# Kernel tuning notes

Measured on AMD Instinct MI355X. Metric: run time of the kernel, lower is better.

The kernel has to match this reference:

```python
import jax, jax.numpy as jnp
import numpy as np

EMBED_DIM = 1024
NUM_HEADS = 16
HEAD_DIM = EMBED_DIM // NUM_HEADS
MLP_HIDDEN = 4096
B, S = 2, 2048


def setup_inputs() -> dict:
    key = jax.random.key(0)
    ks = jax.random.split(key, 10)
    sd = lambda fan_in: 1.0 / np.sqrt(fan_in)
    x = jax.random.normal(ks[0], (B, S, EMBED_DIM), dtype=jnp.float32)
    # weights stored (in, out) so y = x @ W + b (same math as torch Linear)
    w_qkv = jax.random.normal(ks[1], (EMBED_DIM, 3 * EMBED_DIM), jnp.float32) * sd(EMBED_DIM)
    w_proj = jax.random.normal(ks[2], (EMBED_DIM, EMBED_DIM), jnp.float32) * sd(EMBED_DIM)
    b_proj = jnp.zeros((EMBED_DIM,), jnp.float32)
    w_fc1 = jax.random.normal(ks[3], (EMBED_DIM, MLP_HIDDEN), jnp.float32) * sd(EMBED_DIM)
    b_fc1 = jnp.zeros((MLP_HIDDEN,), jnp.float32)
    w_fc2 = jax.random.normal(ks[4], (MLP_HIDDEN, EMBED_DIM), jnp.float32) * sd(MLP_HIDDEN)
    b_fc2 = jnp.zeros((EMBED_DIM,), jnp.float32)
    g1 = jnp.ones((EMBED_DIM,), jnp.float32)
    be1 = jnp.zeros((EMBED_DIM,), jnp.float32)
    g2 = jnp.ones((EMBED_DIM,), jnp.float32)
    be2 = jnp.zeros((EMBED_DIM,), jnp.float32)
    return {"x": x, "w_qkv": w_qkv, "w_proj": w_proj, "b_proj": b_proj,
            "w_fc1": w_fc1, "b_fc1": b_fc1, "w_fc2": w_fc2, "b_fc2": b_fc2,
            "g1": g1, "be1": be1, "g2": g2, "be2": be2}


def _layernorm(x, g, b, eps=1e-5):
    mu = jnp.mean(x, axis=-1, keepdims=True)
    var = jnp.var(x, axis=-1, keepdims=True)
    return (x - mu) * jax.lax.rsqrt(var + eps) * g + b


def _block(x, w_qkv, w_proj, b_proj, w_fc1, b_fc1, w_fc2, b_fc2, g1, be1, g2, be2):
    # --- attention branch ---
    h = _layernorm(x, g1, be1)
    qkv = h @ w_qkv  # [B,S,3D]
    qkv = qkv.reshape(B, S, 3, NUM_HEADS, HEAD_DIM).transpose(2, 0, 3, 1, 4)
    q, k, v = qkv[0], qkv[1], qkv[2]  # each [B,H,S,Dh]
    scale = 1.0 / np.sqrt(HEAD_DIM).astype(np.float32)
    dots = jnp.einsum('bhqd,bhkd->bhqk', q, k) * scale  # naive full score matrix
    attn = jax.nn.softmax(dots, axis=-1)
    out = jnp.einsum('bhqk,bhkd->bhqd', attn, v)
    out = out.transpose(0, 2, 1, 3).reshape(B, S, EMBED_DIM)
    x = x + (out @ w_proj + b_proj)
    # --- mlp branch ---
    h2 = _layernorm(x, g2, be2)
    mlp = jax.nn.gelu(h2 @ w_fc1 + b_fc1, approximate=False) @ w_fc2 + b_fc2
    return x + mlp


def reference(x, w_qkv, w_proj, b_proj, w_fc1, b_fc1, w_fc2, b_fc2, g1, be1, g2, be2):
    return _block(x, w_qkv, w_proj, b_proj, w_fc1, b_fc1, w_fc2, b_fc2, g1, be1, g2, be2)
```

## Files before the change

kernel.cpp:

```cpp
#include <hip/hip_runtime.h>

typedef __attribute__((ext_vector_type(8))) short short8;
typedef __attribute__((ext_vector_type(4))) float f32x4;

#define MFMA16(a, b, c) __builtin_amdgcn_mfma_f32_16x16x32_bf16((a), (b), (c), 0, 0, 0)

static __device__ __forceinline__ unsigned short f2bf(float f) {
    unsigned int u = __float_as_uint(f);
    return (unsigned short)((u + 0x7fffu + ((u >> 16) & 1u)) >> 16);
}

static __device__ __forceinline__ void glds16(const unsigned short* g, unsigned short* l) {
    __builtin_amdgcn_global_load_lds(
        (const __attribute__((address_space(1))) unsigned int*)g,
        (__attribute__((address_space(3))) unsigned int*)l, 16, 0, 0);
}

__global__ __launch_bounds__(256) void convt_all_kernel(
    const float* __restrict__ w_qkv, const float* __restrict__ w_proj,
    const float* __restrict__ w_fc1, const float* __restrict__ w_fc2,
    unsigned short* __restrict__ wqkvT, unsigned short* __restrict__ wprojT,
    unsigned short* __restrict__ wfc1T, unsigned short* __restrict__ wfc2T) {
    __shared__ unsigned short Ts[32][33];
    int id = blockIdx.x;
    const float* W; unsigned short* WT; int K, N, bx, by;
    if (id < 3072)      { W = w_qkv;  WT = wqkvT;  K = 1024; N = 3072; bx = id % 96;  by = id / 96; }
    else if (id < 4096) { id -= 3072; W = w_proj; WT = wprojT; K = 1024; N = 1024; bx = id & 31; by = id >> 5; }
    else if (id < 8192) { id -= 4096; W = w_fc1;  WT = wfc1T;  K = 1024; N = 4096; bx = id & 127; by = id >> 7; }
    else                { id -= 8192; W = w_fc2;  WT = wfc2T;  K = 4096; N = 1024; bx = id & 31; by = id >> 5; }
    int t = threadIdx.x;
    int bk = by * 32, bn = bx * 32;
    int r = t >> 3, c = (t & 7) * 4;
    float4 w = *(const float4*)&W[(size_t)(bk + r) * N + bn + c];
    Ts[c + 0][r] = f2bf(w.x); Ts[c + 1][r] = f2bf(w.y);
    Ts[c + 2][r] = f2bf(w.z); Ts[c + 3][r] = f2bf(w.w);
    __syncthreads();
    ushort4 o;
    o.x = Ts[r][c]; o.y = Ts[r][c + 1]; o.z = Ts[r][c + 2]; o.w = Ts[r][c + 3];
    *(ushort4*)&WT[(size_t)(bn + r) * K + bk + c] = o;
}

__global__ __launch_bounds__(256) void ln_kernel(const float* __restrict__ x,
                                                 const float* __restrict__ g,
                                                 const float* __restrict__ be,
                                                 unsigned short* __restrict__ y) {
    int row = blockIdx.x;
    const float* xr = x + (size_t)row * 1024;
    unsigned short* yr = y + (size_t)row * 1024;
    int t = threadIdx.x;
    float v[4];
    float sum = 0.f, sq = 0.f;
#pragma unroll
    for (int i = 0; i < 4; ++i) {
        float f = xr[t + i * 256];
        v[i] = f; sum += f; sq += f * f;
    }
#pragma unroll
    for (int o = 32; o > 0; o >>= 1) { sum += __shfl_down(sum, o); sq += __shfl_down(sq, o); }
    __shared__ float red[8];
    int wave = t >> 6, lane = t & 63;
    if (lane == 0) { red[wave] = sum; red[4 + wave] = sq; }
    __syncthreads();
    sum = red[0] + red[1] + red[2] + red[3];
    sq  = red[4] + red[5] + red[6] + red[7];
    float mean = sum * (1.f / 1024.f);
    float var  = sq * (1.f / 1024.f) - mean * mean;
    float rstd = rsqrtf(var + 1e-5f);
#pragma unroll
    for (int i = 0; i < 4; ++i) {
        int c = t + i * 256;
        yr[c] = f2bf((v[i] - mean) * rstd * g[c] + be[c]);
    }
}

#define PHASE_MID                                            \
    __builtin_amdgcn_sched_barrier(0);                       \
    __builtin_amdgcn_s_barrier();                            \
    asm volatile("s_waitcnt lgkmcnt(0)" ::: "memory");       \
    __builtin_amdgcn_sched_barrier(0);                       \
    __builtin_amdgcn_s_setprio(1);
#define PHASE_END                                            \
    __builtin_amdgcn_s_setprio(0);                           \
    __builtin_amdgcn_sched_barrier(0);                       \
    __builtin_amdgcn_s_barrier();

__global__ __launch_bounds__(512, 2) void gemm256_kernel(const unsigned short* __restrict__ A,
                                                         const unsigned short* __restrict__ BT,
                                                         const float* __restrict__ bias,
                                                         const float* __restrict__ resid,
                                                         void* __restrict__ C,
                                                         int M, int N, int K, int act, int cF32) {
    __shared__ __align__(16) unsigned short As[2][2][256][32];
    __shared__ __align__(16) unsigned short Bs[2][2][256][32];
    int t = threadIdx.x, wave = t >> 6, lane = t & 63;
    int lm = lane & 15, quad = lane >> 4;
    int wm = (wave >> 2) * 128, wn = (wave & 3) * 64;

    int id = blockIdx.y * gridDim.x + blockIdx.x;
    int gsz = gridDim.x * 8;
    int grp = id / gsz, rem = id % gsz;
    int br = (grp * 8 + (rem & 7)) * 256;
    int bc = (rem >> 3) * 256;

    int srow = lane >> 2;
    int scol = ((lane & 3) ^ ((srow >> 1) & 3)) * 8;
    const unsigned short* Ag = A + (size_t)(br + wave * 16 + srow) * K + scol;
    const unsigned short* Bg = BT + (size_t)(bc + wave * 16 + srow) * K + scol;

    auto stA = [&](int p_, int half, int ko) {
        const unsigned short* g = Ag + (size_t)half * 128 * K + ko;
        glds16(g,      &As[p_][0][half * 128 + wave * 16][0]);
        glds16(g + 32, &As[p_][1][half * 128 + wave * 16][0]);
    };
    auto stB = [&](int p_, int half, int ko) {
        const unsigned short* g = Bg + (size_t)half * 128 * K + ko;
        glds16(g,      &Bs[p_][0][half * 128 + wave * 16][0]);
        glds16(g + 32, &Bs[p_][1][half * 128 + wave * 16][0]);
    };

    f32x4 zero4 = {0.f, 0.f, 0.f, 0.f};
    f32x4 acc[8][4];
#pragma unroll
    for (int i = 0; i < 8; ++i)
#pragma unroll
        for (int j = 0; j < 4; ++j) acc[i][j] = zero4;

    int ntile = K >> 6;
    stA(0, 0, 0); stA(0, 1, 0); stB(0, 0, 0); stB(0, 1, 0);
    if (ntile > 1) { stB(1, 0, 64); stA(1, 0, 64); }
    __builtin_amdgcn_sched_barrier(0);
    if (ntile > 1) asm volatile("s_waitcnt vmcnt(4)" ::: "memory");
    else           asm volatile("s_waitcnt vmcnt(0)" ::: "memory");
    __builtin_amdgcn_s_barrier();

    int cq = (quad ^ ((lm >> 1) & 3)) << 3;

    for (int tt = 0; tt < ntile; ++tt) {
        int p = tt & 1, q = p ^ 1;
        int tko = tt * 64;
        short8 aLo0[4], aLo1[4], bLo0[2], bLo1[2];
#pragma unroll
        for (int i = 0; i < 4; ++i) {
            aLo0[i] = *(const short8*)&As[p][0][wm + i * 16 + lm][cq];
            aLo1[i] = *(const short8*)&As[p][1][wm + i * 16 + lm][cq];
        }
#pragma unroll
        for (int j = 0; j < 2; ++j) {
            bLo0[j] = *(const short8*)&Bs[p][0][wn + j * 16 + lm][cq];
            bLo1[j] = *(const short8*)&Bs[p][1][wn + j * 16 + lm][cq];
        }
        if (tt + 1 < ntile) stB(q, 1, tko + 64);
        PHASE_MID;
#pragma unroll
        for (int i = 0; i < 4; ++i)
#pragma unroll
            for (int j = 0; j < 2; ++j) {
                acc[i][j] = MFMA16(aLo0[i], bLo0[j], acc[i][j]);
                acc[i][j] = MFMA16(aLo1[i], bLo1[j], acc[i][j]);
            }
        PHASE_END;
        short8 bHi0[2], bHi1[2];
#pragma unroll
        for (int j = 0; j < 2; ++j) {
            bHi0[j] = *(const short8*)&Bs[p][0][wn + 32 + j * 16 + lm][cq];
            bHi1[j] = *(const short8*)&Bs[p][1][wn + 32 + j * 16 + lm][cq];
        }
        if (tt + 1 < ntile) stA(q, 1, tko + 64);
        PHASE_MID;
#pragma unroll
        for (int i = 0; i < 4; ++i)
#pragma unroll
            for (int j = 0; j < 2; ++j) {
                acc[i][j + 2] = MFMA16(aLo0[i], bHi0[j], acc[i][j + 2]);
                acc[i][j + 2] = MFMA16(aLo1[i], bHi1[j], acc[i][j + 2]);
            }
        PHASE_END;
        short8 aHi0[4], aHi1[4];
#pragma unroll
        for (int i = 0; i < 4; ++i) {
            aHi0[i] = *(const short8*)&As[p][0][wm + 64 + i * 16 + lm][cq];
            aHi1[i] = *(const short8*)&As[p][1][wm + 64 + i * 16 + lm][cq];
        }
        if (tt + 2 < ntile) stB(p, 0, tko + 128);
        PHASE_MID;
#pragma unroll
        for (int i = 0; i < 4; ++i)
#pragma unroll
            for (int j = 0; j < 2; ++j) {
                acc[i + 4][j] = MFMA16(aHi0[i], bLo0[j], acc[i + 4][j]);
                acc[i + 4][j] = MFMA16(aHi1[i], bLo1[j], acc[i + 4][j]);
            }
        PHASE_END;
        if (tt + 2 < ntile) stA(p, 0, tko + 128);
        __builtin_amdgcn_sched_barrier(0);
        if (tt + 2 < ntile) asm volatile("s_waitcnt vmcnt(4)" ::: "memory");
        else                asm volatile("s_waitcnt vmcnt(0)" ::: "memory");
        __builtin_amdgcn_s_barrier();
        asm volatile("s_waitcnt lgkmcnt(0)" ::: "memory");
        __builtin_amdgcn_sched_barrier(0);
        __builtin_amdgcn_s_setprio(1);
#pragma unroll
        for (int i = 0; i < 4; ++i)
#pragma unroll
            for (int j = 0; j < 2; ++j) {
                acc[i + 4][j + 2] = MFMA16(aHi0[i], bHi0[j], acc[i + 4][j + 2]);
                acc[i + 4][j + 2] = MFMA16(aHi1[i], bHi1[j], acc[i + 4][j + 2]);
            }
        PHASE_END;
    }

#pragma unroll
    for (int i = 0; i < 8; ++i)
#pragma unroll
        for (int j = 0; j < 4; ++j) {
            int col = bc + wn + j * 16 + lm;
            float bv = bias ? bias[col] : 0.f;
#pragma unroll
            for (int r = 0; r < 4; ++r) {
                int row = br + wm + i * 16 + quad * 4 + r;
                float v = acc[i][j][r] + bv;
                if (act == 1) v = 0.5f * v * (1.f + erff(v * 0.70710678118f));
                size_t idx = (size_t)row * N + col;
                if (resid) v += resid[idx];
                if (cF32) ((float*)C)[idx] = v;
                else ((unsigned short*)C)[idx] = f2bf(v);
            }
        }
}

__global__ __launch_bounds__(256) void gemm64_4ph(const unsigned short* __restrict__ A,
                                                  const unsigned short* __restrict__ BT,
                                                  const float* __restrict__ bias,
                                                  const float* __restrict__ resid,
                                                  void* __restrict__ C,
                                                  int M, int N, int K, int act, int cF32) {
    __shared__ __align__(16) unsigned short As[3][2][128][32];
    __shared__ __align__(16) unsigned short Bs[3][2][64][32];
    int t = threadIdx.x, wave = t >> 6, lane = t & 63;
    int lm = lane & 15, quad = lane >> 4;
    int wm = (wave >> 1) * 64, wn = (wave & 1) * 32;

    int id = blockIdx.y * gridDim.x + blockIdx.x;
    int gsz = gridDim.x * 8;
    int grp = id / gsz, rem = id % gsz;
    int br = (grp * 8 + (rem & 7)) * 128;
    int bc = (rem >> 3) * 64;

    int srow = lane >> 2;
    int scol = ((lane & 3) ^ ((srow >> 1) & 3)) * 8;
    const unsigned short* Ag = A + (size_t)(br + wave * 16 + srow) * K + scol;
    const unsigned short* Bg = BT + (size_t)(bc + wave * 16 + srow) * K + scol;

    auto stA = [&](int b, int ko) {
#pragma unroll
        for (int l = 0; l < 4; ++l)
            glds16(Ag + (size_t)(l >> 1) * 64 * K + (l & 1) * 32 + ko,
                   &As[b][l & 1][(l >> 1) * 64 + wave * 16][0]);
    };
    auto stB = [&](int b, int ko) {
#pragma unroll
        for (int l = 0; l < 2; ++l)
            glds16(Bg + (size_t)l * 32 + ko, &Bs[b][l][wave * 16][0]);
    };

    f32x4 zero4 = {0.f, 0.f, 0.f, 0.f};
    f32x4 acc[4][2];
#pragma unroll
    for (int i = 0; i < 4; ++i) { acc[i][0] = zero4; acc[i][1] = zero4; }

    int nt = K >> 6;
    stA(0, 0); stB(0, 0);
    if (nt > 1) { stA(1, 64); stB(1, 64); }
    __builtin_amdgcn_sched_barrier(0);
    if (nt > 1) asm volatile("s_waitcnt vmcnt(6)" ::: "memory");
    else        asm volatile("s_waitcnt vmcnt(0)" ::: "memory");
    __builtin_amdgcn_s_barrier();

    int cq = (quad ^ ((lm >> 1) & 3)) << 3;

    int p = 0;
    for (int tt = 0; tt < nt; ++tt) {
        int pn = p + 1; if (pn == 3) pn = 0;
        int pnn = pn + 1; if (pnn == 3) pnn = 0;
        short8 a0[4], a1[4], b00, b01;
#pragma unroll
        for (int i = 0; i < 4; ++i) {
            a0[i] = *(const short8*)&As[p][0][wm + i * 16 + lm][cq];
            a1[i] = *(const short8*)&As[p][1][wm + i * 16 + lm][cq];
        }
        b00 = *(const short8*)&Bs[p][0][wn + lm][cq];
        b01 = *(const short8*)&Bs[p][1][wn + lm][cq];
        if (tt + 2 < nt) stA(pnn, (tt + 2) << 6);
        PHASE_MID;
#pragma unroll
        for (int i = 0; i < 4; ++i) {
            acc[i][0] = MFMA16(a0[i], b00, acc[i][0]);
            acc[i][0] = MFMA16(a1[i], b01, acc[i][0]);
        }
        PHASE_END;
        short8 b10 = *(const short8*)&Bs[p][0][wn + 16 + lm][cq];
        short8 b11 = *(const short8*)&Bs[p][1][wn + 16 + lm][cq];
        if (tt + 2 < nt) stB(pnn, (tt + 2) << 6);
        __builtin_amdgcn_sched_barrier(0);
        if (tt + 2 < nt) asm volatile("s_waitcnt vmcnt(6)" ::: "memory");
        else             asm volatile("s_waitcnt vmcnt(0)" ::: "memory");
        __builtin_amdgcn_s_barrier();
        asm volatile("s_waitcnt lgkmcnt(0)" ::: "memory");
        __builtin_amdgcn_sched_barrier(0);
        __builtin_amdgcn_s_setprio(1);
#pragma unroll
        for (int i = 0; i < 4; ++i) {
            acc[i][1] = MFMA16(a0[i], b10, acc[i][1]);
            acc[i][1] = MFMA16(a1[i], b11, acc[i][1]);
        }
        PHASE_END;
        p = pn;
    }

#pragma unroll
    for (int i = 0; i < 4; ++i)
#pragma unroll
        for (int j = 0; j < 2; ++j) {
            int col = bc + wn + j * 16 + lm;
            float bv = bias ? bias[col] : 0.f;
#pragma unroll
            for (int r = 0; r < 4; ++r) {
                int row = br + wm + i * 16 + quad * 4 + r;
                float v = acc[i][j][r] + bv;
                if (act == 1) v = 0.5f * v * (1.f + erff(v * 0.70710678118f));
                size_t idx = (size_t)row * N + col;
                if (resid) v += resid[idx];
                if (cF32) ((float*)C)[idx] = v;
                else ((unsigned short*)C)[idx] = f2bf(v);
            }
        }
}

template <int BN>
__global__ __launch_bounds__(256) void gemm_kernel(const unsigned short* __restrict__ A,
                                                   const unsigned short* __restrict__ BT,
                                                   const float* __restrict__ bias,
                                                   const float* __restrict__ resid,
                                                   void* __restrict__ C,
                                                   int M, int N, int K, int act, int cF32) {
    constexpr int NT = BN / 32;
    __shared__ __align__(16) unsigned short As[2][128][32];
    __shared__ __align__(16) unsigned short Bs[2][BN][32];
    int t = threadIdx.x, wave = t >> 6, lane = t & 63;
    int lm = lane & 15, quad = lane >> 4;
    int wm = (wave >> 1) * 64, wn = (wave & 1) * (BN / 2);

    int id = blockIdx.y * gridDim.x + blockIdx.x;
    int gsz = gridDim.x * 8;
    int grp = id / gsz, rem = id % gsz;
    int br = (grp * 8 + (rem & 7)) * 128;
    int bc = (rem >> 3) * BN;

    int srow = lane >> 2;
    int scol = ((lane & 3) ^ ((srow >> 1) & 3)) * 8;
    const unsigned short* Ag0 = A + (size_t)(br + wave * 32 + srow) * K + scol;
    const unsigned short* Ag1 = Ag0 + (size_t)16 * K;
    const unsigned short* Bg0 = BT + (size_t)(bc + wave * (BN / 4) + srow) * K + scol;
    const unsigned short* Bg1 = Bg0 + (size_t)16 * K;

    f32x4 zero4 = {0.f, 0.f, 0.f, 0.f};
    f32x4 acc[4][NT];
#pragma unroll
    for (int i = 0; i < 4; ++i)
#pragma unroll
        for (int j = 0; j < NT; ++j) acc[i][j] = zero4;

    auto stage = [&](int buf, int ko) {
        glds16(Ag0 + ko, &As[buf][wave * 32][0]);
        glds16(Ag1 + ko, &As[buf][wave * 32 + 16][0]);
        glds16(Bg0 + ko, &Bs[buf][wave * (BN / 4)][0]);
        if (BN == 128) glds16(Bg1 + ko, &Bs[buf][wave * (BN / 4) + 16][0]);
    };

    int nt = K >> 5;
    stage(0, 0);
    int rsw = (lm >> 1) & 3;
    int cq = (quad ^ rsw) << 3;
    for (int tt = 0; tt < nt; ++tt) {
        int cur = tt & 1;
        if (tt + 1 < nt) {
            stage(cur ^ 1, (tt + 1) << 5);
            if (BN == 128) asm volatile("s_waitcnt vmcnt(4)" ::: "memory");
            else           asm volatile("s_waitcnt vmcnt(3)" ::: "memory");
        } else {
            asm volatile("s_waitcnt vmcnt(0)" ::: "memory");
        }
        __builtin_amdgcn_s_barrier();
        __builtin_amdgcn_sched_barrier(0);
        short8 af[4], bf[NT];
#pragma unroll
        for (int i = 0; i < 4; ++i) af[i] = *(const short8*)&As[cur][wm + i * 16 + lm][cq];
#pragma unroll
        for (int j = 0; j < NT; ++j) bf[j] = *(const short8*)&Bs[cur][wn + j * 16 + lm][cq];
#pragma unroll
        for (int i = 0; i < 4; ++i)
#pragma unroll
            for (int j = 0; j < NT; ++j) acc[i][j] = MFMA16(af[i], bf[j], acc[i][j]);
        __builtin_amdgcn_sched_barrier(0);
        __builtin_amdgcn_s_barrier();
    }

#pragma unroll
    for (int i = 0; i < 4; ++i)
#pragma unroll
        for (int j = 0; j < NT; ++j) {
            int col = bc + wn + j * 16 + lm;
            float bv = bias ? bias[col] : 0.f;
#pragma unroll
            for (int r = 0; r < 4; ++r) {
                int row = br + wm + i * 16 + quad * 4 + r;
                float v = acc[i][j][r] + bv;
                if (act == 1) v = 0.5f * v * (1.f + erff(v * 0.70710678118f));
                size_t idx = (size_t)row * N + col;
                if (resid) v += resid[idx];
                if (cF32) ((float*)C)[idx] = v;
                else ((unsigned short*)C)[idx] = f2bf(v);
            }
        }
}

__global__ __launch_bounds__(256) void kvprep_kernel(const unsigned short* __restrict__ qkv,
                                                     unsigned short* __restrict__ Kp,
                                                     unsigned short* __restrict__ Vt) {
    __shared__ unsigned short Vl[64][72];
    int t = threadIdx.x;
    int w = blockIdx.x, bh = blockIdx.y;
    int b = bh >> 4, h = bh & 15;
    int kt = w * 64;
    int sl = t >> 2, c = (t & 3) * 16;
    const unsigned short* src = qkv + (size_t)(b * 2048 + kt + sl) * 3072 + h * 64 + c;
    {
        uint4 k0 = *(const uint4*)(src + 1024);
        uint4 k1 = *(const uint4*)(src + 1024 + 8);
        int sw = sl & 7;
        int o0 = (c >> 3), o1 = o0 + 1;
        unsigned short* krow = Kp + ((size_t)bh * 2048 + kt + sl) * 64;
        *(uint4*)&krow[(o0 ^ sw) << 3] = k0;
        *(uint4*)&krow[(o1 ^ sw) << 3] = k1;
    }
    {
        uint4 v0 = *(const uint4*)(src + 2048);
        uint4 v1 = *(const uint4*)(src + 2048 + 8);
        *(uint4*)&Vl[sl][c] = v0;
        *(uint4*)&Vl[sl][c + 8] = v1;
    }
    __syncthreads();
    {
        int d = t >> 2, kc = (t & 3) * 16;
        unsigned short vv[16];
#pragma unroll
        for (int i = 0; i < 16; ++i) vv[i] = Vl[kc + i][d];
        int sw = d & 7;
        int ko0 = kc >> 3, ko1 = ko0 + 1;
        unsigned short* vrow = Vt + ((((size_t)bh * 32 + w) * 64) + d) * 64;
        *(uint4*)&vrow[(ko0 ^ sw) << 3] = *(uint4*)&vv[0];
        *(uint4*)&vrow[(ko1 ^ sw) << 3] = *(uint4*)&vv[8];
    }
}

__global__ __launch_bounds__(256) void attn2_kernel(const unsigned short* __restrict__ qkv,
                                                    const unsigned short* __restrict__ Kp,
                                                    const unsigned short* __restrict__ Vt,
                                                    unsigned short* __restrict__ out) {
    __shared__ __align__(16) unsigned short Qs[64][72];
    __shared__ __align__(16) unsigned short Ks[4096];
    __shared__ __align__(16) unsigned short Vs[4096];
    __shared__ __align__(16) unsigned short Ps[4][16][72];

    int t = threadIdx.x, wave = t >> 6, lane = t & 63;
    int lm = lane & 15, quad = lane >> 4, k8 = quad * 8;
    int bh = blockIdx.y, b = bh >> 4, h = bh & 15;
    int q0 = blockIdx.x * 64;
    const unsigned short* base = qkv + (size_t)b * 2048 * 3072 + h * 64;

    {
        int r = t >> 2, c = (t & 3) * 16;
        const unsigned short* src = base + (size_t)(q0 + r) * 3072 + c;
        *(uint4*)&Qs[r][c] = *(const uint4*)src;
        *(uint4*)&Qs[r][c + 8] = *(const uint4*)(src + 8);
    }
    __syncthreads();
    short8 qa0 = *(const short8*)&Qs[wave * 16 + lm][k8];
    short8 qa1 = *(const short8*)&Qs[wave * 16 + lm][32 + k8];

    f32x4 zero4 = {0.f, 0.f, 0.f, 0.f};
    f32x4 oacc[4] = {zero4, zero4, zero4, zero4};
    float lsum[4] = {0.f, 0.f, 0.f, 0.f};

    for (int kt = 0; kt < 2048; kt += 64) {
        __syncthreads();
        {
            const unsigned short* kg = Kp + ((size_t)bh * 2048 + kt) * 64 + wave * 1024 + (lane << 3);
            unsigned short* kl = &Ks[wave * 1024];
            glds16(kg, kl);
            glds16(kg + 512, kl + 512);
            const unsigned short* vg = Vt + (((size_t)bh * 32 + (kt >> 6)) * 64) * 64 + wave * 1024 + (lane << 3);
            unsigned short* vl = &Vs[wave * 1024];
            glds16(vg, vl);
            glds16(vg + 512, vl + 512);
        }
        __syncthreads();

        f32x4 s[4];
        __builtin_amdgcn_s_setprio(1);
#pragma unroll
        for (int nt = 0; nt < 4; ++nt) {
            int key = nt * 16 + lm;
            int swk = lm & 7;
            const unsigned short* krow = &Ks[key * 64];
            short8 kf0 = *(const short8*)&krow[(quad ^ swk) << 3];
            short8 kf1 = *(const short8*)&krow[((quad ^ swk) ^ 4) << 3];
            f32x4 a = zero4;
            a = MFMA16(qa0, kf0, a);
            a = MFMA16(qa1, kf1, a);
            s[nt] = a;
        }
        __builtin_amdgcn_s_setprio(0);

#pragma unroll
        for (int r = 0; r < 4; ++r) {
            int row = quad * 4 + r;
            int sw = (row >> 1) & 7;
#pragma unroll
            for (int nt = 0; nt < 4; ++nt) {
                float p = __expf(s[nt][r] * 0.125f - 8.0f);
                lsum[r] += p;
                int g = (nt << 1) + (lm >> 3);
                Ps[wave][row][((g ^ sw) << 3) + (lm & 7)] = f2bf(p);
            }
        }

        __builtin_amdgcn_s_setprio(1);
#pragma unroll
        for (int kh = 0; kh < 2; ++kh) {
            int pg = (kh << 2) + quad;
            short8 pa = *(const short8*)&Ps[wave][lm][(pg ^ ((lm >> 1) & 7)) << 3];
#pragma unroll
            for (int nt = 0; nt < 4; ++nt) {
                int d = nt * 16 + lm;
                short8 vf = *(const short8*)&Vs[d * 64 + ((pg ^ (lm & 7)) << 3)];
                oacc[nt] = MFMA16(pa, vf, oacc[nt]);
            }
        }
        __builtin_amdgcn_s_setprio(0);
    }

#pragma unroll
    for (int r = 0; r < 4; ++r) {
        float l = lsum[r];
        l += __shfl_xor(l, 1); l += __shfl_xor(l, 2);
        l += __shfl_xor(l, 4); l += __shfl_xor(l, 8);
        float inv = 1.f / l;
        int qrow = q0 + wave * 16 + quad * 4 + r;
        size_t o = ((size_t)(b * 2048 + qrow)) * 1024 + h * 64;
#pragma unroll
        for (int nt = 0; nt < 4; ++nt) out[o + nt * 16 + lm] = f2bf(oacc[nt][r] * inv);
    }
}

__global__ __launch_bounds__(256) void attn_kernel(const unsigned short* __restrict__ qkv,
                                                   unsigned short* __restrict__ out) {
    __shared__ __align__(16) unsigned short Qs[64][72];
    __shared__ __align__(16) unsigned short Ks[64][72];
    __shared__ __align__(16) unsigned short Vs[64][72];
    __shared__ __align__(16) unsigned short Ps[4][16][72];
    int t = threadIdx.x, wave = t >> 6, lane = t & 63;
    int lm = lane & 15, quad = lane >> 4, k8 = quad * 8;
    int bh = blockIdx.y, b = bh >> 4, h = bh & 15;
    int q0 = blockIdx.x * 64;
    const unsigned short* base = qkv + (size_t)b * 2048 * 3072 + h * 64;
    const unsigned short* kb = base + 1024;
    const unsigned short* vb = base + 2048;
    {
        int r = t >> 2, c = (t & 3) * 16;
        const unsigned short* src = base + (size_t)(q0 + r) * 3072 + c;
        *(uint4*)&Qs[r][c] = *(const uint4*)src;
        *(uint4*)&Qs[r][c + 8] = *(const uint4*)(src + 8);
    }
    __syncthreads();
    short8 qa0 = *(const short8*)&Qs[wave * 16 + lm][k8];
    short8 qa1 = *(const short8*)&Qs[wave * 16 + lm][32 + k8];
    f32x4 zero4 = {0.f, 0.f, 0.f, 0.f};
    f32x4 oacc[4] = {zero4, zero4, zero4, zero4};
    float lsum[4] = {0.f, 0.f, 0.f, 0.f};
    int sr = t >> 2, sc = (t & 3) * 16;
    for (int kt = 0; kt < 2048; kt += 64) {
        __syncthreads();
        {
            const unsigned short* ksrc = kb + (size_t)(kt + sr) * 3072 + sc;
            *(uint4*)&Ks[sr][sc] = *(const uint4*)ksrc;
            *(uint4*)&Ks[sr][sc + 8] = *(const uint4*)(ksrc + 8);
            const unsigned short* vsrc = vb + (size_t)(kt + sr) * 3072 + sc;
            unsigned short tv[16] __attribute__((aligned(16)));
            *(uint4*)&tv[0] = *(const uint4*)vsrc;
            *(uint4*)&tv[8] = *(const uint4*)(vsrc + 8);
            int kg = sr >> 3, kw = sr & 7;
#pragma unroll
            for (int j = 0; j < 16; ++j) {
                int d = sc + j;
                Vs[d][((kg ^ ((d >> 3) & 7)) << 3) + kw] = tv[j];
            }
        }
        __syncthreads();
        f32x4 s[4];
#pragma unroll
        for (int nt = 0; nt < 4; ++nt) {
            short8 kf0 = *(const short8*)&Ks[nt * 16 + lm][k8];
            short8 kf1 = *(const short8*)&Ks[nt * 16 + lm][32 + k8];
            f32x4 a = zero4;
            a = MFMA16(qa0, kf0, a);
            a = MFMA16(qa1, kf1, a);
            s[nt] = a;
        }
#pragma unroll
        for (int r = 0; r < 4; ++r) {
            int row = quad * 4 + r;
            int sw = (row >> 1) & 7;
#pragma unroll
            for (int nt = 0; nt < 4; ++nt) {
                float p = __expf(s[nt][r] * 0.125f - 8.0f);
                lsum[r] += p;
                int g = (nt << 1) + (lm >> 3);
                Ps[wave][row][((g ^ sw) << 3) + (lm & 7)] = f2bf(p);
            }
        }
#pragma unroll
        for (int kh = 0; kh < 2; ++kh) {
            int pg = (kh << 2) + quad;
            short8 pa = *(const short8*)&Ps[wave][lm][(pg ^ ((lm >> 1) & 7)) << 3];
#pragma unroll
            for (int nt = 0; nt < 4; ++nt) {
                int d = nt * 16 + lm;
                short8 vf = *(const short8*)&Vs[d][(pg ^ ((d >> 3) & 7)) << 3];
                oacc[nt] = MFMA16(pa, vf, oacc[nt]);
            }
        }
    }
#pragma unroll
    for (int r = 0; r < 4; ++r) {
        float l = lsum[r];
        l += __shfl_xor(l, 1); l += __shfl_xor(l, 2);
        l += __shfl_xor(l, 4); l += __shfl_xor(l, 8);
        float inv = 1.f / l;
        int qrow = q0 + wave * 16 + quad * 4 + r;
        size_t o = ((size_t)(b * 2048 + qrow)) * 1024 + h * 64;
#pragma unroll
        for (int nt = 0; nt < 4; ++nt) out[o + nt * 16 + lm] = f2bf(oacc[nt][r] * inv);
    }
}

extern "C" void kernel_launch(void* const* d_in, const int* in_sizes, int n_in,
                              void* d_out, int out_size, void* d_ws, size_t ws_size,
                              hipStream_t stream) {
    const float* x      = (const float*)d_in[0];
    const float* w_qkv  = (const float*)d_in[1];
    const float* w_proj = (const float*)d_in[2];
    const float* b_proj = (const float*)d_in[3];
    const float* w_fc1  = (const float*)d_in[4];
    const float* b_fc1  = (const float*)d_in[5];
    const float* w_fc2  = (const float*)d_in[6];
    const float* b_fc2  = (const float*)d_in[7];
    const float* g1     = (const float*)d_in[8];
    const float* be1    = (const float*)d_in[9];
    const float* g2     = (const float*)d_in[10];
    const float* be2    = (const float*)d_in[11];
    float* out = (float*)d_out;
    unsigned short* sb = (unsigned short*)d_out;

    char* ws = (char*)d_ws;
    unsigned short* wqkvT  = (unsigned short*)ws;
    unsigned short* wprojT = (unsigned short*)(ws + ((size_t)6u << 20));
    unsigned short* wfc1T  = (unsigned short*)(ws + ((size_t)8u << 20));
    unsigned short* wfc2T  = (unsigned short*)(ws + ((size_t)16u << 20));
    unsigned short* qkv    = (unsigned short*)(ws + ((size_t)24u << 20));

    convt_all_kernel<<<dim3(12288), dim3(256), 0, stream>>>(
        w_qkv, w_proj, w_fc1, w_fc2, wqkvT, wprojT, wfc1T, wfc2T);
    ln_kernel<<<dim3(4096), dim3(256), 0, stream>>>(x, g1, be1, sb);
    gemm256_kernel<<<dim3(12, 16), dim3(512), 0, stream>>>(
        sb, wqkvT, nullptr, nullptr, qkv, 4096, 3072, 1024, 0, 0);

    if (ws_size >= ((size_t)72u << 20)) {
        unsigned short* Kp = (unsigned short*)(ws + ((size_t)48u << 20));
        unsigned short* Vt = (unsigned short*)(ws + ((size_t)56u << 20));
        float*          x2 = (float*)(ws + ((size_t)24u << 20));
        unsigned short* m1 = (unsigned short*)(ws + ((size_t)40u << 20));
        kvprep_kernel<<<dim3(32, 32), dim3(256), 0, stream>>>(qkv, Kp, Vt);
        attn2_kernel<<<dim3(32, 32), dim3(256), 0, stream>>>(qkv, Kp, Vt, sb);
        gemm64_4ph<<<dim3(16, 32), dim3(256), 0, stream>>>(
            sb, wprojT, b_proj, x, x2, 4096, 1024, 1024, 0, 1);
        ln_kernel<<<dim3(4096), dim3(256), 0, stream>>>(x2, g2, be2, sb);
        gemm256_kernel<<<dim3(16, 16), dim3(512), 0, stream>>>(
            sb, wfc1T, b_fc1, nullptr, m1, 4096, 4096, 1024, 1, 0);
        gemm64_4ph<<<dim3(16, 32), dim3(256), 0, stream>>>(
            m1, wfc2T, b_fc2, x2, out, 4096, 1024, 4096, 0, 1);
    } else {
        float*          x2  = (float*)(ws + ((size_t)24u << 20));
        unsigned short* m1c = (unsigned short*)(ws + ((size_t)40u << 20));
        unsigned short* h2  = (unsigned short*)d_out + ((size_t)4u << 20);
        attn_kernel<<<dim3(32, 32), dim3(256), 0, stream>>>(qkv, sb);
        gemm_kernel<64><<<dim3(16, 32), dim3(256), 0, stream>>>(
            sb, wprojT, b_proj, x, x2, 4096, 1024, 1024, 0, 1);
        ln_kernel<<<dim3(4096), dim3(256), 0, stream>>>(x2, g2, be2, h2);
        for (int c = 0; c < 4; ++c) {
            size_t ro = (size_t)c * 1024;
            gemm_kernel<128><<<dim3(32, 8), dim3(256), 0, stream>>>(
                h2 + ro * 1024, wfc1T, b_fc1, nullptr, m1c, 1024, 4096, 1024, 1, 0);
            gemm_kernel<64><<<dim3(16, 8), dim3(256), 0, stream>>>(
                m1c, wfc2T, b_fc2, x2 + ro * 1024, out + ro * 1024, 1024, 1024, 4096, 0, 1);
        }
    }
}
```

Baseline: 396.3 us.

## Replace 256x256 GEMM with 128x256 triple-buffered K=32 pipeline for QKV and FC1

Replaces the 256x256-tile, K=64 four-phase GEMM with a 128x256 tile that walks K in steps of 32 through a three-stage LDS ring. Each iteration issues a single prefetch two stages ahead and runs one MFMA block. Smaller tiles double the block count (192 to 384 for QKV, 256 to 512 for FC1) so the grid fills the CUs better, and launch bounds allow 4 blocks per CU. The cost is less operand reuse per tile and more barriers per unit of K.

```diff
diff --git a/kernel.cpp b/kernel.cpp
--- a/kernel.cpp
+++ b/kernel.cpp
@@ -84,117 +84,65 @@
     __builtin_amdgcn_sched_barrier(0);                       \
     __builtin_amdgcn_s_barrier();
 
-__global__ __launch_bounds__(512, 2) void gemm256_kernel(const unsigned short* __restrict__ A,
-                                                         const unsigned short* __restrict__ BT,
-                                                         const float* __restrict__ bias,
-                                                         const float* __restrict__ resid,
-                                                         void* __restrict__ C,
-                                                         int M, int N, int K, int act, int cF32) {
-    __shared__ __align__(16) unsigned short As[2][2][256][32];
-    __shared__ __align__(16) unsigned short Bs[2][2][256][32];
+__global__ __launch_bounds__(512, 4) void gemm128x256_kernel(
+    const unsigned short* __restrict__ A, const unsigned short* __restrict__ BT,
+    const float* __restrict__ bias, const float* __restrict__ resid,
+    void* __restrict__ C, int M, int N, int K, int act, int cF32) {
+    __shared__ __align__(16) unsigned short As[3][128][32];
+    __shared__ __align__(16) unsigned short Bs[3][256][32];
     int t = threadIdx.x, wave = t >> 6, lane = t & 63;
     int lm = lane & 15, quad = lane >> 4;
-    int wm = (wave >> 2) * 128, wn = (wave & 3) * 64;
+    int wm = (wave >> 2) * 64, wn = (wave & 3) * 64;
 
     int id = blockIdx.y * gridDim.x + blockIdx.x;
     int gsz = gridDim.x * 8;
     int grp = id / gsz, rem = id % gsz;
-    int br = (grp * 8 + (rem & 7)) * 256;
+    int br = (grp * 8 + (rem & 7)) * 128;
     int bc = (rem >> 3) * 256;
 
     int srow = lane >> 2;
     int scol = ((lane & 3) ^ ((srow >> 1) & 3)) * 8;
     const unsigned short* Ag = A + (size_t)(br + wave * 16 + srow) * K + scol;
-    const unsigned short* Bg = BT + (size_t)(bc + wave * 16 + srow) * K + scol;
-
-    auto stA = [&](int p_, int half, int ko) {
-        const unsigned short* g = Ag + (size_t)half * 128 * K + ko;
-        glds16(g,      &As[p_][0][half * 128 + wave * 16][0]);
-        glds16(g + 32, &As[p_][1][half * 128 + wave * 16][0]);
+    const unsigned short* Bg = BT + (size_t)(bc + wave * 32 + srow) * K + scol;
+
+    auto stage = [&](int b, int ko) {
+        glds16(Ag + ko, &As[b][wave * 16][0]);
+        glds16(Bg + ko, &Bs[b][wave * 32][0]);
+        glds16(Bg + (size_t)16 * K + ko, &Bs[b][wave * 32 + 16][0]);
     };
-    auto stB = [&](int p_, int half, int ko) {
-        const unsigned short* g = Bg + (size_t)half * 128 * K + ko;
-        glds16(g,      &Bs[p_][0][half * 128 + wave * 16][0]);
-        glds16(g + 32, &Bs[p_][1][half * 128 + wave * 16][0]);
-    };
 
     f32x4 zero4 = {0.f, 0.f, 0.f, 0.f};
-    f32x4 acc[8][4];
-#pragma unroll
-    for (int i = 0; i < 8; ++i)
+    f32x4 acc[4][4];
+#pragma unroll
+    for (int i = 0; i < 4; ++i)
 #pragma unroll
         for (int j = 0; j < 4; ++j) acc[i][j] = zero4;
 
-    int ntile = K >> 6;
-    stA(0, 0, 0); stA(0, 1, 0); stB(0, 0, 0); stB(0, 1, 0);
-    if (ntile > 1) { stB(1, 0, 64); stA(1, 0, 64); }
+    int nt = K >> 5;
+    stage(0, 0);
+    stage(1, 32);
     __builtin_amdgcn_sched_barrier(0);
-    if (ntile > 1) asm volatile("s_waitcnt vmcnt(4)" ::: "memory");
-    else           asm volatile("s_waitcnt vmcnt(0)" ::: "memory");
+    asm volatile("s_waitcnt vmcnt(3)" ::: "memory");
     __builtin_amdgcn_s_barrier();
 
     int cq = (quad ^ ((lm >> 1) & 3)) << 3;
 
-    for (int tt = 0; tt < ntile; ++tt) {
-        int p = tt & 1, q = p ^ 1;
-        int tko = tt * 64;
-        short8 aLo0[4], aLo1[4], bLo0[2], bLo1[2];
-#pragma unroll
-        for (int i = 0; i < 4; ++i) {
-            aLo0[i] = *(const short8*)&As[p][0][wm + i * 16 + lm][cq];
-            aLo1[i] = *(const short8*)&As[p][1][wm + i * 16 + lm][cq];
-        }
-#pragma unroll
-        for (int j = 0; j < 2; ++j) {
-            bLo0[j] = *(const short8*)&Bs[p][0][wn + j * 16 + lm][cq];
-            bLo1[j] = *(const short8*)&Bs[p][1][wn + j * 16 + lm][cq];
-        }
-        if (tt + 1 < ntile) stB(q, 1, tko + 64);
-        PHASE_MID;
-#pragma unroll
-        for (int i = 0; i < 4; ++i)
-#pragma unroll
-            for (int j = 0; j < 2; ++j) {
-                acc[i][j] = MFMA16(aLo0[i], bLo0[j], acc[i][j]);
-                acc[i][j] = MFMA16(aLo1[i], bLo1[j], acc[i][j]);
-            }
-        PHASE_END;
-        short8 bHi0[2], bHi1[2];
-#pragma unroll
-        for (int j = 0; j < 2; ++j) {
-            bHi0[j] = *(const short8*)&Bs[p][0][wn + 32 + j * 16 + lm][cq];
-            bHi1[j] = *(const short8*)&Bs[p][1][wn + 32 + j * 16 + lm][cq];
-        }
-        if (tt + 1 < ntile) stA(q, 1, tko + 64);
-        PHASE_MID;
-#pragma unroll
-        for (int i = 0; i < 4; ++i)
-#pragma unroll
-            for (int j = 0; j < 2; ++j) {
-                acc[i][j + 2] = MFMA16(aLo0[i], bHi0[j], acc[i][j + 2]);
-                acc[i][j + 2] = MFMA16(aLo1[i], bHi1[j], acc[i][j + 2]);
-            }
-        PHASE_END;
-        short8 aHi0[4], aHi1[4];
-#pragma unroll
-        for (int i = 0; i < 4; ++i) {
-            aHi0[i] = *(const short8*)&As[p][0][wm + 64 + i * 16 + lm][cq];
-            aHi1[i] = *(const short8*)&As[p][1][wm + 64 + i * 16 + lm][cq];
-        }
-        if (tt + 2 < ntile) stB(p, 0, tko + 128);
-        PHASE_MID;
-#pragma unroll
-        for (int i = 0; i < 4; ++i)
-#pragma unroll
-            for (int j = 0; j < 2; ++j) {
-                acc[i + 4][j] = MFMA16(aHi0[i], bLo0[j], acc[i + 4][j]);
-                acc[i + 4][j] = MFMA16(aHi1[i], bLo1[j], acc[i + 4][j]);
-            }
-        PHASE_END;
-        if (tt + 2 < ntile) stA(p, 0, tko + 128);
-        __builtin_amdgcn_sched_barrier(0);
-        if (tt + 2 < ntile) asm volatile("s_waitcnt vmcnt(4)" ::: "memory");
-        else                asm volatile("s_waitcnt vmcnt(0)" ::: "memory");
+    int p = 0;
+    for (int tt = 0; tt < nt; ++tt) {
+        int pnn = p + 2; if (pnn >= 3) pnn -= 3;
+        short8 af[4], bf[4];
+#pragma unroll
+        for (int i = 0; i < 4; ++i) af[i] = *(const short8*)&As[p][wm + i * 16 + lm][cq];
+#pragma unroll
+        for (int j = 0; j < 4; ++j) bf[j] = *(const short8*)&Bs[p][wn + j * 16 + lm][cq];
+        if (tt + 2 < nt) {
+            stage(pnn, (tt + 2) << 5);
+            __builtin_amdgcn_sched_barrier(0);
+            asm volatile("s_waitcnt vmcnt(3)" ::: "memory");
+        } else {
+            __builtin_amdgcn_sched_barrier(0);
+            asm volatile("s_waitcnt vmcnt(0)" ::: "memory");
+        }
         __builtin_amdgcn_s_barrier();
         asm volatile("s_waitcnt lgkmcnt(0)" ::: "memory");
         __builtin_amdgcn_sched_barrier(0);
@@ -202,15 +150,13 @@
 #pragma unroll
         for (int i = 0; i < 4; ++i)
 #pragma unroll
-            for (int j = 0; j < 2; ++j) {
-                acc[i + 4][j + 2] = MFMA16(aHi0[i], bHi0[j], acc[i + 4][j + 2]);
-                acc[i + 4][j + 2] = MFMA16(aHi1[i], bHi1[j], acc[i + 4][j + 2]);
-            }
+            for (int j = 0; j < 4; ++j) acc[i][j] = MFMA16(af[i], bf[j], acc[i][j]);
         PHASE_END;
-    }
-
-#pragma unroll
-    for (int i = 0; i < 8; ++i)
+        p = p + 1; if (p == 3) p = 0;
+    }
+
+#pragma unroll
+    for (int i = 0; i < 4; ++i)
 #pragma unroll
         for (int j = 0; j < 4; ++j) {
             int col = bc + wn + j * 16 + lm;
@@ -682,7 +628,7 @@
     convt_all_kernel<<<dim3(12288), dim3(256), 0, stream>>>(
         w_qkv, w_proj, w_fc1, w_fc2, wqkvT, wprojT, wfc1T, wfc2T);
     ln_kernel<<<dim3(4096), dim3(256), 0, stream>>>(x, g1, be1, sb);
-    gemm256_kernel<<<dim3(12, 16), dim3(512), 0, stream>>>(
+    gemm128x256_kernel<<<dim3(12, 32), dim3(512), 0, stream>>>(
         sb, wqkvT, nullptr, nullptr, qkv, 4096, 3072, 1024, 0, 0);
 
     if (ws_size >= ((size_t)72u << 20)) {
@@ -695,7 +641,7 @@
         gemm64_4ph<<<dim3(16, 32), dim3(256), 0, stream>>>(
             sb, wprojT, b_proj, x, x2, 4096, 1024, 1024, 0, 1);
         ln_kernel<<<dim3(4096), dim3(256), 0, stream>>>(x2, g2, be2, sb);
-        gemm256_kernel<<<dim3(16, 16), dim3(512), 0, stream>>>(
+        gemm128x256_kernel<<<dim3(16, 32), dim3(512), 0, stream>>>(
             sb, wfc1T, b_fc1, nullptr, m1, 4096, 4096, 1024, 1, 0);
         gemm64_4ph<<<dim3(16, 32), dim3(256), 0, stream>>>(
             m1, wfc2T, b_fc2, x2, out, 4096, 1024, 4096, 0, 1);
```

After: 370.7 us. 6.5% less time.
